# Kernel tuning notes

Hardware: AMD Instinct MI355X
Metric: run time of the kernel (lower is better)

## Reference

```python
import jax, jax.numpy as jnp
import numpy as np

B, S, D, H = 8, 2048, 768, 768

def setup_inputs() -> dict:
    key = jax.random.key(0)
    ks = jax.random.split(key, 8)
    s = 1.0 / np.sqrt(D)
    return {
        "x": jax.random.normal(ks[0], (B, S, D), dtype=jnp.float32),
        "y": jax.random.normal(ks[1], (B, S, D), dtype=jnp.float32),
        "Wq": jax.random.uniform(ks[2], (D, H), jnp.float32, -s, s),
        "bq": jax.random.uniform(ks[3], (H,), jnp.float32, -s, s),
        "Wk": jax.random.uniform(ks[4], (D, H), jnp.float32, -s, s),
        "bk": jax.random.uniform(ks[5], (H,), jnp.float32, -s, s),
        "Wv": jax.random.uniform(ks[6], (D, H), jnp.float32, -s, s),
        "bv": jax.random.uniform(ks[7], (H,), jnp.float32, -s, s),
    }

def reference(x, y, Wq, bq, Wk, bk, Wv, bv):
    q = jnp.einsum('bsd,dh->bsh', x, Wq) + bq      # [B,S,H]
    k = jnp.einsum('bsd,dh->bsh', x, Wk) + bk      # [B,S,H]
    v = jnp.einsum('bsd,dh->bsh', y, Wv) + bv      # [B,S,H]
    scores = jnp.einsum('bqh,bkh->bqk', q, k)      # [B,S,S], no scaling in original
    probs = jax.nn.softmax(scores, axis=-1)
    bilinear_v = q * v                              # elementwise gate
    context = jnp.einsum('bqk,bkh->bqh', probs, bilinear_v)
    return context  # dropout is identity in eval mode
```

## Files before the change

kernel.cpp:

```cpp
#include <hip/hip_runtime.h>
#include <cstdint>
#include <cstddef>


#define BM 128
#define BN 128
#define BK 32

using half8 = __attribute__((ext_vector_type(8))) _Float16;
using half4 = __attribute__((ext_vector_type(4))) _Float16;
using f32x4 = __attribute__((ext_vector_type(4))) float;

__global__ __launch_bounds__(256) void cvt2_f32_f16(
    const float* __restrict__ a, const float* __restrict__ b,
    _Float16* __restrict__ oa, _Float16* __restrict__ ob, int n4) {
  const float* in = blockIdx.y ? b : a;
  _Float16* out = blockIdx.y ? ob : oa;
  int i = blockIdx.x * 256 + threadIdx.x;
  if (i >= n4) return;
  float4 v = ((const float4*)in)[i];
  half4 o = {(_Float16)v.x, (_Float16)v.y, (_Float16)v.z, (_Float16)v.w};
  *(half4*)&out[(size_t)i * 4] = o;
}

__global__ __launch_bounds__(256) void tr3_cvt768(
    const float* __restrict__ Wq, const float* __restrict__ Wk,
    const float* __restrict__ Wv, _Float16* __restrict__ Wt) {
  const float* W = (blockIdx.y == 0) ? Wq : (blockIdx.y == 1) ? Wk : Wv;
  _Float16* o = Wt + (size_t)blockIdx.y * 589824;
  int i = blockIdx.x * 256 + threadIdx.x;
  int h = i / 768, d = i - h * 768;
  o[i] = (_Float16)W[d * 768 + h];
}

template <int MODE>
__global__ __launch_bounds__(256) void gemm_bt(
    const _Float16* __restrict__ Ab, int ldA, long sA,
    const _Float16* __restrict__ Bb, int ldB, long sB,
    void* __restrict__ Cb, int ldc, long sC,
    int K, const float* __restrict__ bias, const _Float16* __restrict__ qb,
    const float* __restrict__ bias2, void* __restrict__ Cb2) {
  __shared__ __align__(16) _Float16 lA[BM * BK];
  __shared__ __align__(16) _Float16 lB[BN * BK];

  const int tid  = threadIdx.x;
  const int lane = tid & 63;
  const int quad = lane >> 4;
  const int l15  = lane & 15;
  const int wave = tid >> 6;
  const int wm = (wave >> 1) * 64;
  const int wn = (wave & 1) * 64;
  const long bm = (long)blockIdx.x * BM;
  const long bn = (long)blockIdx.y * BN;
  const _Float16* A = Ab + (long)blockIdx.z * sA;
  const _Float16* B = Bb + (long)blockIdx.z * sB;

  f32x4 acc[4][4] = {};

  const int c0 = tid,        r0 = c0 >> 2, k0c = (c0 & 3) * 8;
  const int c1 = 256 + tid,  r1 = c1 >> 2, k1c = (c1 & 3) * 8;
  const _Float16* gA0 = A + (size_t)(bm + r0) * ldA + k0c;
  const _Float16* gA1 = A + (size_t)(bm + r1) * ldA + k1c;
  const _Float16* gB0 = B + (size_t)(bn + r0) * ldB + k0c;
  const _Float16* gB1 = B + (size_t)(bn + r1) * ldB + k1c;

  for (int kk = 0; kk < K; kk += BK) {
    __syncthreads();
    __builtin_amdgcn_global_load_lds(
        (const __attribute__((address_space(1))) void*)(gA0 + kk),
        (__attribute__((address_space(3))) void*)&lA[c0 * 8], 16, 0, 0);
    __builtin_amdgcn_global_load_lds(
        (const __attribute__((address_space(1))) void*)(gA1 + kk),
        (__attribute__((address_space(3))) void*)&lA[c1 * 8], 16, 0, 0);
    __builtin_amdgcn_global_load_lds(
        (const __attribute__((address_space(1))) void*)(gB0 + kk),
        (__attribute__((address_space(3))) void*)&lB[c0 * 8], 16, 0, 0);
    __builtin_amdgcn_global_load_lds(
        (const __attribute__((address_space(1))) void*)(gB1 + kk),
        (__attribute__((address_space(3))) void*)&lB[c1 * 8], 16, 0, 0);
    __syncthreads();

    half8 af[4], bfr[4];
#pragma unroll
    for (int i = 0; i < 4; i++) {
      af[i]  = *(const half8*)&lA[(wm + i * 16 + l15) * BK + quad * 8];
      bfr[i] = *(const half8*)&lB[(wn + i * 16 + l15) * BK + quad * 8];
    }
#pragma unroll
    for (int i = 0; i < 4; i++)
#pragma unroll
      for (int j = 0; j < 4; j++)
        acc[i][j] = __builtin_amdgcn_mfma_f32_16x16x32_f16(
            af[i], bfr[j], acc[i][j], 0, 0, 0);
  }

  if constexpr (MODE == 1) {
    __shared__ __align__(16) _Float16 xp[4 * 32 * 72];
    _Float16* xw = &xp[wave * 2304];
    const long sbase = (bm & 2047) + wm;
    const long bb = bm >> 11;
    const long hbase = bn + wn;
#pragma unroll
    for (int jh = 0; jh < 2; jh++) {
      __syncthreads();
#pragma unroll
      for (int j2 = 0; j2 < 2; j2++) {
        const int j = jh * 2 + j2;
        const long n_g = hbase + j * 16 + l15;
        const float bsv = bias[n_g];
#pragma unroll
        for (int i = 0; i < 4; i++) {
          half4 pk;
#pragma unroll
          for (int r = 0; r < 4; r++) {
            long m_g = bm + wm + i * 16 + quad * 4 + r;
            float v = acc[i][j][r] + bsv;
            float q = (float)qb[m_g * (long)ldc + n_g];
            pk[r] = (_Float16)(v * q);
          }
          *(half4*)&xw[(j2 * 16 + l15) * 72 + i * 16 + quad * 4] = pk;
        }
      }
      __syncthreads();
#pragma unroll
      for (int t = 0; t < 4; t++) {
        const int n_r = t * 8 + (lane >> 3);
        const int m8 = (lane & 7) * 8;
        half8 vv = *(const half8*)&xw[n_r * 72 + m8];
        *(half8*)&((_Float16*)Cb)[(bb * 768 + hbase + 32 * jh + n_r) * 2048 +
                                  sbase + m8] = vv;
      }
    }
  } else {
#pragma unroll
    for (int i = 0; i < 4; i++) {
#pragma unroll
      for (int j = 0; j < 4; j++) {
#pragma unroll
        for (int r = 0; r < 4; r++) {
          long m = bm + wm + i * 16 + quad * 4 + r;
          long n = bn + wn + j * 16 + l15;
          float v = acc[i][j][r];
          if constexpr (MODE == 3) {
            const bool isq = (bn < 768);
            long nn = isq ? n : n - 768;
            v += (isq ? bias : bias2)[nn];
            _Float16* dst = (_Float16*)(isq ? Cb : Cb2);
            dst[m * ldc + nn] = (_Float16)v;
          } else {
            ((float*)Cb + (long)blockIdx.z * sC)[m * ldc + n] = v;
          }
        }
      }
    }
  }
}

__global__ __launch_bounds__(512, 2) void gemm256(
    const _Float16* __restrict__ Ab, int ldA, long sA,
    const _Float16* __restrict__ Bb, int ldB, long sB,
    float* __restrict__ Cb, int ldc, long sC, int K) {
  __shared__ __align__(16) _Float16 lds[8][8192];

  const int tid  = threadIdx.x;
  const int lane = tid & 63;
  const int l15  = lane & 15;
  const int quad = lane >> 4;
  const int wave = tid >> 6;
  const int wmi  = wave >> 2;
  const int wni  = wave & 3;

  const int cpx = gridDim.x >> 3;
  const int l   = blockIdx.x;
  const int nl  = (l & 7) * cpx + (l >> 3);
  const long bm = (long)(nl & 7) * 256;
  const long bn = (long)(nl >> 3) * 256;

  const _Float16* A = Ab + (long)blockIdx.y * sA;
  const _Float16* B = Bb + (long)blockIdx.y * sB;
  float* C = Cb + (long)blockIdx.y * sC;

  const int srow = tid >> 3;
  const int scol = ((tid & 7) ^ (srow & 7)) * 8;
  const _Float16* gA = A + (bm + srow) * (long)ldA + scol;
  const _Float16* gB = B + (bn + srow) * (long)ldB + scol;

#define STAGE(op, GP, LD, buf, half, kt)                                       \
  { const _Float16* s0_ = (GP) + (long)(half) * 128 * (LD) + (long)(kt) * 64;  \
    _Float16* d0_ = &lds[(buf) * 4 + (op) * 2 + (half)][tid * 8];              \
    __builtin_amdgcn_global_load_lds(                                          \
        (const __attribute__((address_space(1))) void*)s0_,                    \
        (__attribute__((address_space(3))) void*)d0_, 16, 0, 0);               \
    __builtin_amdgcn_global_load_lds(                                          \
        (const __attribute__((address_space(1))) void*)(s0_ + 64 * (long)(LD)),\
        (__attribute__((address_space(3))) void*)(d0_ + 4096), 16, 0, 0); }

  const int NT = K >> 6;
  f32x4 acc[8][4] = {};

  STAGE(1, gB, ldB, 0, 0, 0)
  STAGE(1, gB, ldB, 0, 1, 0)
  STAGE(0, gA, ldA, 0, 0, 0)
  STAGE(0, gA, ldA, 0, 1, 0)
  STAGE(1, gB, ldB, 1, 0, 1)
  STAGE(1, gB, ldB, 1, 1, 1)
  asm volatile("s_waitcnt vmcnt(4)" ::: "memory");
  __builtin_amdgcn_s_barrier();
  asm volatile("" ::: "memory");

  const int sw4 = (l15 & 7) << 4;
  const int rB0 = (wni & 1) * 64;
  half8 bf[4][2];

  for (int kt = 0; kt < NT; ++kt) {
    const int b = kt & 1;
    const char* lA = (const char*)lds[b * 4 + wmi];
    const char* lB = (const char*)lds[b * 4 + 2 + (wni >> 1)];
#pragma unroll
    for (int ph = 0; ph < 4; ++ph) {
      half8 af[2][2];
#pragma unroll
      for (int i2 = 0; i2 < 2; ++i2)
#pragma unroll
        for (int ks = 0; ks < 2; ++ks)
          af[i2][ks] = *(const half8*)(lA + (((ph * 2 + i2) * 16 + l15) * 128 +
                                             ((((ks << 2) | quad) << 4) ^ sw4)));
      if (ph == 0) {
#pragma unroll
        for (int j = 0; j < 4; ++j)
#pragma unroll
          for (int ks = 0; ks < 2; ++ks)
            bf[j][ks] = *(const half8*)(lB + ((rB0 + j * 16 + l15) * 128 +
                                              ((((ks << 2) | quad) << 4) ^ sw4)));
      }
      if (ph == 0 && kt + 1 < NT) STAGE(0, gA, ldA, b ^ 1, 0, kt + 1)
      if (ph == 1 && kt + 1 < NT) STAGE(0, gA, ldA, b ^ 1, 1, kt + 1)
      if (ph == 2 && kt + 2 < NT) STAGE(1, gB, ldB, b, 0, kt + 2)
      if (ph == 3 && kt + 2 < NT) STAGE(1, gB, ldB, b, 1, kt + 2)
      asm volatile("" ::: "memory");
      __builtin_amdgcn_s_barrier();
      asm volatile("" ::: "memory");
      __builtin_amdgcn_s_setprio(1);
#pragma unroll
      for (int i2 = 0; i2 < 2; ++i2)
#pragma unroll
        for (int j = 0; j < 4; ++j)
#pragma unroll
          for (int ks = 0; ks < 2; ++ks)
            acc[ph * 2 + i2][j] = __builtin_amdgcn_mfma_f32_16x16x32_f16(
                af[i2][ks], bf[j][ks], acc[ph * 2 + i2][j], 0, 0, 0);
      __builtin_amdgcn_s_setprio(0);
      if (ph == 3) {
        if (kt < NT - 2) {
          asm volatile("s_waitcnt vmcnt(4)" ::: "memory");
        } else if (kt == NT - 2) {
          asm volatile("s_waitcnt vmcnt(0)" ::: "memory");
        }
      }
      asm volatile("" ::: "memory");
      __builtin_amdgcn_s_barrier();
      asm volatile("" ::: "memory");
    }
  }
#undef STAGE

  float* Cp = C + (bm + wmi * 128 + quad * 4) * (long)ldc + bn + wni * 64 + l15;
#pragma unroll
  for (int i = 0; i < 8; ++i)
#pragma unroll
    for (int j = 0; j < 4; ++j)
#pragma unroll
      for (int r = 0; r < 4; ++r)
        Cp[(i * 16 + r) * (long)ldc + j * 16] = acc[i][j][r];
}

__global__ __launch_bounds__(256) void softmax_rows(
    const float* __restrict__ sc, _Float16* __restrict__ pr, int prPitch) {
  const int row = blockIdx.x;
  const float* x = sc + (size_t)row * 2048;
  const int t = threadIdx.x;
  float4 v0 = ((const float4*)x)[2 * t];
  float4 v1 = ((const float4*)x)[2 * t + 1];
  float e[8] = {v0.x, v0.y, v0.z, v0.w, v1.x, v1.y, v1.z, v1.w};

  float m = e[0];
#pragma unroll
  for (int i = 1; i < 8; i++) m = fmaxf(m, e[i]);
#pragma unroll
  for (int o = 32; o; o >>= 1) m = fmaxf(m, __shfl_xor(m, o, 64));
  __shared__ float red[4];
  if ((t & 63) == 0) red[t >> 6] = m;
  __syncthreads();
  m = fmaxf(fmaxf(red[0], red[1]), fmaxf(red[2], red[3]));

  float s = 0.f;
#pragma unroll
  for (int i = 0; i < 8; i++) { e[i] = __expf(e[i] - m); s += e[i]; }
#pragma unroll
  for (int o = 32; o; o >>= 1) s += __shfl_xor(s, o, 64);
  __syncthreads();
  if ((t & 63) == 0) red[t >> 6] = s;
  __syncthreads();
  s = red[0] + red[1] + red[2] + red[3];
  float inv = 1.0f / s;

  union { _Float16 h[8]; uint4 v; } o;
#pragma unroll
  for (int i = 0; i < 8; i++) o.h[i] = (_Float16)(e[i] * inv);
  ((uint4*)(pr + (size_t)row * prPitch))[t] = o.v;
}

extern "C" void kernel_launch(void* const* d_in, const int* in_sizes, int n_in,
                              void* d_out, int out_size, void* d_ws, size_t ws_size,
                              hipStream_t stream) {
  const float* x  = (const float*)d_in[0];
  const float* y  = (const float*)d_in[1];
  const float* Wq = (const float*)d_in[2];
  const float* bq = (const float*)d_in[3];
  const float* Wk = (const float*)d_in[4];
  const float* bk = (const float*)d_in[5];
  const float* Wv = (const float*)d_in[6];
  const float* bv = (const float*)d_in[7];
  float* out = (float*)d_out;

  const int S = 2048, D = 768, H = 768;
  const long SH = (long)S * H;
  char* ws = (char*)d_ws;
  _Float16* qb  = (_Float16*)(ws + 0);
  _Float16* kb  = (_Float16*)(ws + 25165824);
  _Float16* gT  = (_Float16*)(ws + 50331648);
  _Float16* xb  = (_Float16*)(ws + 75497472);
  _Float16* yb  = (_Float16*)(ws + 100663296);
  _Float16* WtQ = (_Float16*)(ws + 125829120);
  _Float16* WtV = WtQ + 2 * 589824;
  float* scores = (float*)(ws + 75497472);

  cvt2_f32_f16<<<dim3(12288, 2), 256, 0, stream>>>(x, y, xb, yb, 3145728);
  tr3_cvt768<<<dim3(2304, 3), 256, 0, stream>>>(Wq, Wk, Wv, WtQ);

  gemm_bt<3><<<dim3(128, 12, 1), 256, 0, stream>>>(
      xb, D, 0, WtQ, D, 0, qb, H, 0, D, bq, nullptr, bk, kb);
  gemm_bt<1><<<dim3(128, 6, 1), 256, 0, stream>>>(
      yb, D, 0, WtV, D, 0, gT, H, 0, D, bv, qb, nullptr, nullptr);

  _Float16* probs = (_Float16*)scores;
  if (ws_size >= 209715200ull) {
    gemm256<<<dim3(64, 8), 512, 0, stream>>>(
        qb, H, SH, kb, H, SH, scores, S, (long)S * S, D);
    softmax_rows<<<16384, 256, 0, stream>>>(scores, probs, 4096);
    gemm256<<<dim3(24, 8), 512, 0, stream>>>(
        probs, 4096, (long)S * 4096, gT, S, SH, out, H, SH, S);
  } else {
    for (int r = 0; r < 4; r++) {
      const long b0 = 2 * r;
      gemm256<<<dim3(64, 2), 512, 0, stream>>>(
          qb + b0 * SH, H, SH, kb + b0 * SH, H, SH, scores, S, (long)S * S, D);
      softmax_rows<<<4096, 256, 0, stream>>>(scores, probs, 4096);
      gemm256<<<dim3(24, 2), 512, 0, stream>>>(
          probs, 4096, (long)S * 4096, gT + b0 * SH, S, SH,
          out + b0 * SH, H, SH, S);
    }
  }
}
```

Baseline: 409.7 us.

## Restructure GEMM mainloop into quadrant ping-pong with register double-buffered fragments

Result: no change. 412.5 us (+0.7%).

```diff
diff --git a/kernel.cpp b/kernel.cpp
--- a/kernel.cpp
+++ b/kernel.cpp
@@ -196,71 +196,143 @@
         (__attribute__((address_space(3))) void*)(d0_ + 4096), 16, 0, 0); }
 
   const int NT = K >> 6;
-  f32x4 acc[8][4] = {};
-
-  STAGE(1, gB, ldB, 0, 0, 0)
-  STAGE(1, gB, ldB, 0, 1, 0)
-  STAGE(0, gA, ldA, 0, 0, 0)
-  STAGE(0, gA, ldA, 0, 1, 0)
-  STAGE(1, gB, ldB, 1, 0, 1)
-  STAGE(1, gB, ldB, 1, 1, 1)
-  asm volatile("s_waitcnt vmcnt(4)" ::: "memory");
-  __builtin_amdgcn_s_barrier();
-  asm volatile("" ::: "memory");
-
   const int sw4 = (l15 & 7) << 4;
   const int rB0 = (wni & 1) * 64;
-  half8 bf[4][2];
+
+  f32x4 acc[8][4] = {};
+  half8 af0[8], afB[8], bf0[4], bfB[4];
+
+  STAGE(0, gA, ldA, 0, 0, 0) STAGE(0, gA, ldA, 0, 1, 0)
+  STAGE(1, gB, ldB, 0, 0, 0) STAGE(1, gB, ldB, 0, 1, 0)
+  STAGE(0, gA, ldA, 1, 0, 1) STAGE(0, gA, ldA, 1, 1, 1)
+  STAGE(1, gB, ldB, 1, 0, 1) STAGE(1, gB, ldB, 1, 1, 1)
+  asm volatile("s_waitcnt vmcnt(8)" ::: "memory");
+  __builtin_amdgcn_s_barrier();
+  __builtin_amdgcn_sched_barrier(0);
+
+  {
+    const char* lA = (const char*)lds[wmi];
+    const char* lB = (const char*)lds[2 + (wni >> 1)];
+#pragma unroll
+    for (int i2 = 0; i2 < 4; ++i2)
+#pragma unroll
+      for (int ks = 0; ks < 2; ++ks)
+        af0[i2 * 2 + ks] = *(const half8*)(lA + ((i2 * 16 + l15) * 128 +
+                                           ((((ks << 2) | quad) << 4) ^ sw4)));
+#pragma unroll
+    for (int j2 = 0; j2 < 2; ++j2)
+#pragma unroll
+      for (int ks = 0; ks < 2; ++ks)
+        bf0[j2 * 2 + ks] = *(const half8*)(lB + ((rB0 + j2 * 16 + l15) * 128 +
+                                           ((((ks << 2) | quad) << 4) ^ sw4)));
+    asm volatile("s_waitcnt lgkmcnt(0)" ::: "memory");
+    __builtin_amdgcn_s_barrier();
+    __builtin_amdgcn_sched_barrier(0);
+  }
 
   for (int kt = 0; kt < NT; ++kt) {
     const int b = kt & 1;
-    const char* lA = (const char*)lds[b * 4 + wmi];
-    const char* lB = (const char*)lds[b * 4 + 2 + (wni >> 1)];
-#pragma unroll
-    for (int ph = 0; ph < 4; ++ph) {
-      half8 af[2][2];
-#pragma unroll
-      for (int i2 = 0; i2 < 2; ++i2)
-#pragma unroll
-        for (int ks = 0; ks < 2; ++ks)
-          af[i2][ks] = *(const half8*)(lA + (((ph * 2 + i2) * 16 + l15) * 128 +
+    const char* lA  = (const char*)lds[b * 4 + wmi];
+    const char* lB  = (const char*)lds[b * 4 + 2 + (wni >> 1)];
+    const char* lAn = (const char*)lds[(b ^ 1) * 4 + wmi];
+    const char* lBn = (const char*)lds[(b ^ 1) * 4 + 2 + (wni >> 1)];
+
+#pragma unroll
+    for (int j2 = 0; j2 < 2; ++j2)
+#pragma unroll
+      for (int ks = 0; ks < 2; ++ks)
+        bfB[j2 * 2 + ks] = *(const half8*)(lB + ((rB0 + 32 + j2 * 16 + l15) * 128 +
+                                           ((((ks << 2) | quad) << 4) ^ sw4)));
+    __builtin_amdgcn_s_setprio(1);
+#pragma unroll
+    for (int i2 = 0; i2 < 4; ++i2)
+#pragma unroll
+      for (int j2 = 0; j2 < 2; ++j2)
+#pragma unroll
+        for (int ks = 0; ks < 2; ++ks)
+          acc[i2][j2] = __builtin_amdgcn_mfma_f32_16x16x32_f16(
+              af0[i2 * 2 + ks], bf0[j2 * 2 + ks], acc[i2][j2], 0, 0, 0);
+    __builtin_amdgcn_s_setprio(0);
+    asm volatile("s_waitcnt lgkmcnt(0)" ::: "memory");
+    __builtin_amdgcn_s_barrier();
+    __builtin_amdgcn_sched_barrier(0);
+
+#pragma unroll
+    for (int i2 = 0; i2 < 4; ++i2)
+#pragma unroll
+      for (int ks = 0; ks < 2; ++ks)
+        afB[i2 * 2 + ks] = *(const half8*)(lA + ((64 + i2 * 16 + l15) * 128 +
+                                           ((((ks << 2) | quad) << 4) ^ sw4)));
+    if (kt + 2 < NT) {
+      STAGE(1, gB, ldB, b, 0, kt + 2)
+      STAGE(1, gB, ldB, b, 1, kt + 2)
+    }
+    __builtin_amdgcn_s_setprio(1);
+#pragma unroll
+    for (int i2 = 0; i2 < 4; ++i2)
+#pragma unroll
+      for (int j2 = 0; j2 < 2; ++j2)
+#pragma unroll
+        for (int ks = 0; ks < 2; ++ks)
+          acc[i2][2 + j2] = __builtin_amdgcn_mfma_f32_16x16x32_f16(
+              af0[i2 * 2 + ks], bfB[j2 * 2 + ks], acc[i2][2 + j2], 0, 0, 0);
+    __builtin_amdgcn_s_setprio(0);
+    asm volatile("s_waitcnt lgkmcnt(0)" ::: "memory");
+    if (kt + 2 < NT) {
+      asm volatile("s_waitcnt vmcnt(4)" ::: "memory");
+    } else if (kt + 1 < NT) {
+      asm volatile("s_waitcnt vmcnt(0)" ::: "memory");
+    }
+    __builtin_amdgcn_s_barrier();
+    __builtin_amdgcn_sched_barrier(0);
+
+    if (kt + 2 < NT) {
+      STAGE(0, gA, ldA, b, 0, kt + 2)
+      STAGE(0, gA, ldA, b, 1, kt + 2)
+    }
+    __builtin_amdgcn_s_setprio(1);
+#pragma unroll
+    for (int i2 = 0; i2 < 4; ++i2)
+#pragma unroll
+      for (int j2 = 0; j2 < 2; ++j2)
+#pragma unroll
+        for (int ks = 0; ks < 2; ++ks)
+          acc[4 + i2][j2] = __builtin_amdgcn_mfma_f32_16x16x32_f16(
+              afB[i2 * 2 + ks], bf0[j2 * 2 + ks], acc[4 + i2][j2], 0, 0, 0);
+    __builtin_amdgcn_s_setprio(0);
+    if (kt + 1 < NT) {
+#pragma unroll
+      for (int j2 = 0; j2 < 2; ++j2)
+#pragma unroll
+        for (int ks = 0; ks < 2; ++ks)
+          bf0[j2 * 2 + ks] = *(const half8*)(lBn + ((rB0 + j2 * 16 + l15) * 128 +
                                              ((((ks << 2) | quad) << 4) ^ sw4)));
-      if (ph == 0) {
-#pragma unroll
-        for (int j = 0; j < 4; ++j)
-#pragma unroll
-          for (int ks = 0; ks < 2; ++ks)
-            bf[j][ks] = *(const half8*)(lB + ((rB0 + j * 16 + l15) * 128 +
-                                              ((((ks << 2) | quad) << 4) ^ sw4)));
-      }
-      if (ph == 0 && kt + 1 < NT) STAGE(0, gA, ldA, b ^ 1, 0, kt + 1)
-      if (ph == 1 && kt + 1 < NT) STAGE(0, gA, ldA, b ^ 1, 1, kt + 1)
-      if (ph == 2 && kt + 2 < NT) STAGE(1, gB, ldB, b, 0, kt + 2)
-      if (ph == 3 && kt + 2 < NT) STAGE(1, gB, ldB, b, 1, kt + 2)
-      asm volatile("" ::: "memory");
-      __builtin_amdgcn_s_barrier();
-      asm volatile("" ::: "memory");
-      __builtin_amdgcn_s_setprio(1);
-#pragma unroll
-      for (int i2 = 0; i2 < 2; ++i2)
-#pragma unroll
-        for (int j = 0; j < 4; ++j)
-#pragma unroll
-          for (int ks = 0; ks < 2; ++ks)
-            acc[ph * 2 + i2][j] = __builtin_amdgcn_mfma_f32_16x16x32_f16(
-                af[i2][ks], bf[j][ks], acc[ph * 2 + i2][j], 0, 0, 0);
-      __builtin_amdgcn_s_setprio(0);
-      if (ph == 3) {
-        if (kt < NT - 2) {
-          asm volatile("s_waitcnt vmcnt(4)" ::: "memory");
-        } else if (kt == NT - 2) {
-          asm volatile("s_waitcnt vmcnt(0)" ::: "memory");
-        }
-      }
-      asm volatile("" ::: "memory");
-      __builtin_amdgcn_s_barrier();
-      asm volatile("" ::: "memory");
-    }
+    }
+    asm volatile("s_waitcnt lgkmcnt(0)" ::: "memory");
+    __builtin_amdgcn_s_barrier();
+    __builtin_amdgcn_sched_barrier(0);
+
+    __builtin_amdgcn_s_setprio(1);
+#pragma unroll
+    for (int i2 = 0; i2 < 4; ++i2)
+#pragma unroll
+      for (int j2 = 0; j2 < 2; ++j2)
+#pragma unroll
+        for (int ks = 0; ks < 2; ++ks)
+          acc[4 + i2][2 + j2] = __builtin_amdgcn_mfma_f32_16x16x32_f16(
+              afB[i2 * 2 + ks], bfB[j2 * 2 + ks], acc[4 + i2][2 + j2], 0, 0, 0);
+    __builtin_amdgcn_s_setprio(0);
+    if (kt + 1 < NT) {
+#pragma unroll
+      for (int i2 = 0; i2 < 4; ++i2)
+#pragma unroll
+        for (int ks = 0; ks < 2; ++ks)
+          af0[i2 * 2 + ks] = *(const half8*)(lAn + ((i2 * 16 + l15) * 128 +
+                                             ((((ks << 2) | quad) << 4) ^ sw4)));
+    }
+    asm volatile("s_waitcnt lgkmcnt(0)" ::: "memory");
+    __builtin_amdgcn_s_barrier();
+    __builtin_amdgcn_sched_barrier(0);
   }
 #undef STAGE
 
```

## Load A fragments directly from global into registers in gemm256, stage only B in LDS

Applied to the files above, without the earlier changes.

Result: slower. 550.4 us (+34.4%).

```diff
diff --git a/kernel.cpp b/kernel.cpp
--- a/kernel.cpp
+++ b/kernel.cpp
@@ -160,7 +160,7 @@
     const _Float16* __restrict__ Ab, int ldA, long sA,
     const _Float16* __restrict__ Bb, int ldB, long sB,
     float* __restrict__ Cb, int ldc, long sC, int K) {
-  __shared__ __align__(16) _Float16 lds[8][8192];
+  __shared__ __align__(16) _Float16 ldsB[4][8192];
 
   const int tid  = threadIdx.x;
   const int lane = tid & 63;
@@ -180,89 +180,103 @@
   const _Float16* B = Bb + (long)blockIdx.y * sB;
   float* C = Cb + (long)blockIdx.y * sC;
 
+  const _Float16* aBase = A + (bm + wmi * 128) * (long)ldA;
+  const int aLane = l15 * ldA + quad * 8;
+
   const int srow = tid >> 3;
   const int scol = ((tid & 7) ^ (srow & 7)) * 8;
-  const _Float16* gA = A + (bm + srow) * (long)ldA + scol;
   const _Float16* gB = B + (bn + srow) * (long)ldB + scol;
 
-#define STAGE(op, GP, LD, buf, half, kt)                                       \
-  { const _Float16* s0_ = (GP) + (long)(half) * 128 * (LD) + (long)(kt) * 64;  \
-    _Float16* d0_ = &lds[(buf) * 4 + (op) * 2 + (half)][tid * 8];              \
+#define STAGEB(buf, half, kt)                                                  \
+  { const _Float16* s0_ = gB + (long)(half) * 128 * ldB + (long)(kt) * 64;     \
+    _Float16* d0_ = &ldsB[(buf) * 2 + (half)][tid * 8];                        \
     __builtin_amdgcn_global_load_lds(                                          \
         (const __attribute__((address_space(1))) void*)s0_,                    \
         (__attribute__((address_space(3))) void*)d0_, 16, 0, 0);               \
     __builtin_amdgcn_global_load_lds(                                          \
-        (const __attribute__((address_space(1))) void*)(s0_ + 64 * (long)(LD)),\
+        (const __attribute__((address_space(1))) void*)(s0_ + 64 * (long)ldB), \
         (__attribute__((address_space(3))) void*)(d0_ + 4096), 16, 0, 0); }
 
+#define LOADA(dst, hrow, kt)                                                   \
+  _Pragma("unroll")                                                            \
+  for (int i2 = 0; i2 < 4; ++i2)                                               \
+    _Pragma("unroll")                                                          \
+    for (int ks = 0; ks < 2; ++ks)                                             \
+      dst[i2 * 2 + ks] = *(const half8*)(aBase +                               \
+          (long)(((hrow) + i2 * 16) * ldA + (kt) * 64 + ks * 32) + aLane);
+
+#define RDB(dst, lbuf, roff)                                                   \
+  _Pragma("unroll")                                                            \
+  for (int j2 = 0; j2 < 2; ++j2)                                               \
+    _Pragma("unroll")                                                          \
+    for (int ks = 0; ks < 2; ++ks)                                             \
+      dst[j2 * 2 + ks] = *(const half8*)((lbuf) +                              \
+          (((roff) + j2 * 16 + l15) * 128 + ((((ks << 2) | quad) << 4) ^ sw4)));
+
+#define MFMAQ(iq, jq, afr, bfr)                                                \
+  __builtin_amdgcn_s_setprio(1);                                               \
+  _Pragma("unroll")                                                            \
+  for (int i2 = 0; i2 < 4; ++i2)                                               \
+    _Pragma("unroll")                                                          \
+    for (int j2 = 0; j2 < 2; ++j2)                                             \
+      _Pragma("unroll")                                                        \
+      for (int ks = 0; ks < 2; ++ks)                                           \
+        acc[(iq) * 4 + i2][(jq) * 2 + j2] =                                    \
+            __builtin_amdgcn_mfma_f32_16x16x32_f16(                            \
+                afr[i2 * 2 + ks], bfr[j2 * 2 + ks],                            \
+                acc[(iq) * 4 + i2][(jq) * 2 + j2], 0, 0, 0);                   \
+  __builtin_amdgcn_s_setprio(0);
+
   const int NT = K >> 6;
-  f32x4 acc[8][4] = {};
-
-  STAGE(1, gB, ldB, 0, 0, 0)
-  STAGE(1, gB, ldB, 0, 1, 0)
-  STAGE(0, gA, ldA, 0, 0, 0)
-  STAGE(0, gA, ldA, 0, 1, 0)
-  STAGE(1, gB, ldB, 1, 0, 1)
-  STAGE(1, gB, ldB, 1, 1, 1)
-  asm volatile("s_waitcnt vmcnt(4)" ::: "memory");
-  __builtin_amdgcn_s_barrier();
-  asm volatile("" ::: "memory");
-
   const int sw4 = (l15 & 7) << 4;
   const int rB0 = (wni & 1) * 64;
-  half8 bf[4][2];
+
+  f32x4 acc[8][4] = {};
+  half8 af0[8], afB[8], bf0[4], bfB[4];
+
+  STAGEB(0, 0, 0) STAGEB(0, 1, 0)
+  STAGEB(1, 0, 1) STAGEB(1, 1, 1)
+  LOADA(af0, 0, 0)
+  asm volatile("s_waitcnt vmcnt(12)" ::: "memory");
+  __builtin_amdgcn_s_barrier();
+  __builtin_amdgcn_sched_barrier(0);
+  {
+    const char* lB0 = (const char*)ldsB[(wni >> 1)];
+    RDB(bf0, lB0, rB0)
+  }
 
   for (int kt = 0; kt < NT; ++kt) {
     const int b = kt & 1;
-    const char* lA = (const char*)lds[b * 4 + wmi];
-    const char* lB = (const char*)lds[b * 4 + 2 + (wni >> 1)];
-#pragma unroll
-    for (int ph = 0; ph < 4; ++ph) {
-      half8 af[2][2];
-#pragma unroll
-      for (int i2 = 0; i2 < 2; ++i2)
-#pragma unroll
-        for (int ks = 0; ks < 2; ++ks)
-          af[i2][ks] = *(const half8*)(lA + (((ph * 2 + i2) * 16 + l15) * 128 +
-                                             ((((ks << 2) | quad) << 4) ^ sw4)));
-      if (ph == 0) {
-#pragma unroll
-        for (int j = 0; j < 4; ++j)
-#pragma unroll
-          for (int ks = 0; ks < 2; ++ks)
-            bf[j][ks] = *(const half8*)(lB + ((rB0 + j * 16 + l15) * 128 +
-                                              ((((ks << 2) | quad) << 4) ^ sw4)));
-      }
-      if (ph == 0 && kt + 1 < NT) STAGE(0, gA, ldA, b ^ 1, 0, kt + 1)
-      if (ph == 1 && kt + 1 < NT) STAGE(0, gA, ldA, b ^ 1, 1, kt + 1)
-      if (ph == 2 && kt + 2 < NT) STAGE(1, gB, ldB, b, 0, kt + 2)
-      if (ph == 3 && kt + 2 < NT) STAGE(1, gB, ldB, b, 1, kt + 2)
-      asm volatile("" ::: "memory");
-      __builtin_amdgcn_s_barrier();
-      asm volatile("" ::: "memory");
-      __builtin_amdgcn_s_setprio(1);
-#pragma unroll
-      for (int i2 = 0; i2 < 2; ++i2)
-#pragma unroll
-        for (int j = 0; j < 4; ++j)
-#pragma unroll
-          for (int ks = 0; ks < 2; ++ks)
-            acc[ph * 2 + i2][j] = __builtin_amdgcn_mfma_f32_16x16x32_f16(
-                af[i2][ks], bf[j][ks], acc[ph * 2 + i2][j], 0, 0, 0);
-      __builtin_amdgcn_s_setprio(0);
-      if (ph == 3) {
-        if (kt < NT - 2) {
-          asm volatile("s_waitcnt vmcnt(4)" ::: "memory");
-        } else if (kt == NT - 2) {
-          asm volatile("s_waitcnt vmcnt(0)" ::: "memory");
-        }
-      }
-      asm volatile("" ::: "memory");
-      __builtin_amdgcn_s_barrier();
-      asm volatile("" ::: "memory");
-    }
-  }
-#undef STAGE
+    const char* lB  = (const char*)ldsB[b * 2 + (wni >> 1)];
+    const char* lBn = (const char*)ldsB[(b ^ 1) * 2 + (wni >> 1)];
+
+    LOADA(afB, 64, kt)
+    RDB(bfB, lB, rB0 + 32)
+    MFMAQ(0, 0, af0, bf0)
+    __builtin_amdgcn_sched_barrier(0);
+
+    MFMAQ(0, 1, af0, bfB)
+    if (kt + 2 < NT) {
+      asm volatile("s_waitcnt vmcnt(8) lgkmcnt(0)" ::: "memory");
+    } else {
+      asm volatile("s_waitcnt vmcnt(0) lgkmcnt(0)" ::: "memory");
+    }
+    __builtin_amdgcn_s_barrier();
+    __builtin_amdgcn_sched_barrier(0);
+
+    if (kt + 1 < NT) { LOADA(af0, 0, kt + 1) }
+    if (kt + 2 < NT) { STAGEB(b, 0, kt + 2) STAGEB(b, 1, kt + 2) }
+    MFMAQ(1, 0, afB, bf0)
+    if (kt + 1 < NT) { RDB(bf0, lBn, rB0) }
+    __builtin_amdgcn_sched_barrier(0);
+
+    MFMAQ(1, 1, afB, bfB)
+    __builtin_amdgcn_sched_barrier(0);
+  }
+#undef STAGEB
+#undef LOADA
+#undef RDB
+#undef MFMAQ
 
   float* Cp = C + (bm + wmi * 128 + quad * 4) * (long)ldc + bn + wni * 64 + l15;
 #pragma unroll
```
